# Performance work log

Measured on AMD Instinct MI355X. Metric: run time of the kernel, lower is better.

The kernel has to match this reference:

```python
import jax, jax.numpy as jnp
import numpy as np

INTERMEDIATE = 11008  # weight.size(0)
HIDDEN = 4096         # weight.size(1)
REMAINED = 4403       # int(11008 * 0.4)
BATCH = 64


def setup_inputs() -> dict:
    key = jax.random.key(0)
    k1, k2, k3 = jax.random.split(key, 3)
    x = jax.random.normal(k1, (BATCH, 1, HIDDEN), dtype=jnp.float32)
    weight = jax.random.normal(k2, (INTERMEDIATE, HIDDEN), dtype=jnp.float32) * 0.02
    indices = jax.random.randint(k3, (REMAINED,), 0, INTERMEDIATE, dtype=jnp.int32)
    return {"x": x, "weight": weight, "indices": indices}


def reference(x, weight, indices):
    # Decode path of UpLayer.forward: gather the activation-predicted neuron
    # rows into filtered_W, then x @ filtered_W.T  -> [B, 1, REMAINED]
    filtered_w = weight[indices]                      # [REMAINED, HIDDEN]
    return jnp.einsum('bsh,nh->bsn', x, filtered_w)   # [B, 1, REMAINED]
```

## Files before the change

kernel.cpp:

```cpp
#include <hip/hip_runtime.h>
#include <hip/hip_bf16.h>


#define HIDDEN 4096
#define KSPLIT 8
#define KCHUNK (HIDDEN / KSPLIT)
#define KSTEPS (KCHUNK / 32)
#define BATCH  64
#define NTILE  32
#define XBF_OFF (16u << 20)

using short8  = __attribute__((ext_vector_type(8))) short;
using f32x4   = __attribute__((ext_vector_type(4))) float;

__device__ __forceinline__ short f2bf(float f) {
    __bf16 h = (__bf16)f;
    return __builtin_bit_cast(short, h);
}

__global__ __launch_bounds__(256) void cvt_x(
    const float* __restrict__ x, unsigned short* __restrict__ xbf)
{
    const int i = (blockIdx.x * 256 + threadIdx.x) * 8;
    f32x4 a = *(const f32x4*)(x + i);
    f32x4 b = *(const f32x4*)(x + i + 4);
    short8 h;
    h[0] = f2bf(a[0]); h[1] = f2bf(a[1]); h[2] = f2bf(a[2]); h[3] = f2bf(a[3]);
    h[4] = f2bf(b[0]); h[5] = f2bf(b[1]); h[6] = f2bf(b[2]); h[7] = f2bf(b[3]);
    *(short8*)(xbf + i) = h;
}

__global__ __launch_bounds__(256, 4) void up_gather_gemm(
    const float*          __restrict__ weight,
    const unsigned short* __restrict__ xbf,
    const int*            __restrict__ indices,
    float*                __restrict__ ws,
    int R)
{
    __shared__ unsigned short wlds[NTILE * KCHUNK];

    const int t    = threadIdx.x;
    const int lane = t & 63;
    const int wave = t >> 6;
    const int nl   = lane & 15;
    const int kg   = lane >> 4;
    const int nb   = blockIdx.x;
    const int kb   = blockIdx.y;

    {
        const int r   = t >> 3;
        const int c   = t & 7;
        const int n   = nb * NTILE + r;
        const int row = indices[n < R ? n : R - 1];
        const float* src = weight + (size_t)row * HIDDEN + kb * KCHUNK + c * 8;
        char* ldsrow = (char*)wlds + r * (KCHUNK * 2);
        const unsigned int swz = (unsigned int)((r & 7) << 4);
#pragma unroll
        for (int s = 0; s < 8; ++s) {
            f32x4 v0 = *(const f32x4*)(src + (size_t)s * 64);
            f32x4 v1 = *(const f32x4*)(src + (size_t)s * 64 + 4);
            short8 h;
            h[0] = f2bf(v0[0]); h[1] = f2bf(v0[1]); h[2] = f2bf(v0[2]); h[3] = f2bf(v0[3]);
            h[4] = f2bf(v1[0]); h[5] = f2bf(v1[1]); h[6] = f2bf(v1[2]); h[7] = f2bf(v1[3]);
            const unsigned int bc = (unsigned int)(c * 16 + s * 128);
            *(short8*)(ldsrow + (bc ^ swz)) = h;
        }
    }

    const unsigned short* xrow =
        xbf + (size_t)(wave * 16 + nl) * HIDDEN + kb * KCHUNK + kg * 8;
    short8 afr[KSTEPS];
#pragma unroll
    for (int ks = 0; ks < KSTEPS; ++ks)
        afr[ks] = *(const short8*)(xrow + ks * 32);

    __syncthreads();

    f32x4 acc0 = {0.f,0.f,0.f,0.f}, acc1 = {0.f,0.f,0.f,0.f};

#pragma unroll
    for (int ks = 0; ks < KSTEPS; ++ks) {
#pragma unroll
        for (int nf = 0; nf < 2; ++nf) {
            const int rr = nf * 16 + nl;
            const unsigned int bc =
                (unsigned int)(ks * 64 + kg * 16) ^ (unsigned int)((rr & 7) << 4);
            short8 b = *(const short8*)((const char*)wlds + rr * (KCHUNK * 2) + bc);
            f32x4& acc = nf == 0 ? acc0 : acc1;
            acc = __builtin_amdgcn_mfma_f32_16x16x32_bf16(afr[ks], b, acc, 0, 0, 0);
        }
    }

    float* part = ws + (size_t)kb * BATCH * R;
    f32x4 accs[2] = {acc0, acc1};
#pragma unroll
    for (int nf = 0; nf < 2; ++nf) {
        const int nn = nb * NTILE + nf * 16 + nl;
        if (nn < R) {
#pragma unroll
            for (int r = 0; r < 4; ++r) {
                const int brow = wave * 16 + kg * 4 + r;
                part[(size_t)brow * R + nn] = accs[nf][r];
            }
        }
    }
}

__global__ __launch_bounds__(256) void reduce_partials(
    const float* __restrict__ ws, float* __restrict__ out, int n4, int stride4)
{
    const int i = blockIdx.x * blockDim.x + threadIdx.x;
    if (i >= n4) return;
    const f32x4* w = (const f32x4*)ws;
    f32x4 s = w[i];
#pragma unroll
    for (int kb = 1; kb < KSPLIT; ++kb) {
        f32x4 v = w[(size_t)kb * stride4 + i];
        s[0] += v[0]; s[1] += v[1]; s[2] += v[2]; s[3] += v[3];
    }
    ((f32x4*)out)[i] = s;
}

extern "C" void kernel_launch(void* const* d_in, const int* in_sizes, int n_in,
                              void* d_out, int out_size, void* d_ws, size_t ws_size,
                              hipStream_t stream) {
    const float* x       = (const float*)d_in[0];
    const float* weight  = (const float*)d_in[1];
    const int*   indices = (const int*)d_in[2];
    float*       out     = (float*)d_out;
    float*       ws      = (float*)d_ws;
    unsigned short* xbf  = (unsigned short*)((char*)d_ws + XBF_OFF);

    const int R  = in_sizes[2];
    const int nb = (R + NTILE - 1) / NTILE;

    cvt_x<<<dim3((BATCH * HIDDEN) / (256 * 8)), dim3(256), 0, stream>>>(x, xbf);
    up_gather_gemm<<<dim3(nb, KSPLIT), dim3(256), 0, stream>>>(weight, xbf, indices, ws, R);

    const int n4 = (BATCH * R) / 4;
    reduce_partials<<<dim3((n4 + 255) / 256), dim3(256), 0, stream>>>(ws, out, n4, n4);
}
```

Measured before the change: 32.45 us.

## Halve K-split and software-pipeline two K sub-chunks through registers

KSPLIT goes from 8 to 4, so each block covers 1024 K elements, processed as two 512-wide sub-chunks. The second sub-chunk's weight loads are issued into registers before the first chunk's MFMAs, overlapping global latency with compute. Halving the split also halves the partial-sum workspace that reduce_partials reads. The cost is fewer blocks (half the grid), higher register pressure (launch bounds lowered to 2), and an extra barrier pair.

```diff
diff --git a/kernel.cpp b/kernel.cpp
--- a/kernel.cpp
+++ b/kernel.cpp
@@ -3,19 +3,27 @@
 
 
 #define HIDDEN 4096
-#define KSPLIT 8
+#define KSPLIT 4
 #define KCHUNK (HIDDEN / KSPLIT)
-#define KSTEPS (KCHUNK / 32)
+#define SUB    512
+#define SSTEPS (SUB / 32)
 #define BATCH  64
 #define NTILE  32
 #define XBF_OFF (16u << 20)
 
-using short8  = __attribute__((ext_vector_type(8))) short;
-using f32x4   = __attribute__((ext_vector_type(4))) float;
+using short8 = __attribute__((ext_vector_type(8))) short;
+using f32x4  = __attribute__((ext_vector_type(4))) float;
 
 __device__ __forceinline__ short f2bf(float f) {
     __bf16 h = (__bf16)f;
     return __builtin_bit_cast(short, h);
+}
+
+__device__ __forceinline__ short8 cvt8(const f32x4& lo, const f32x4& hi) {
+    short8 r;
+    r[0] = f2bf(lo[0]); r[1] = f2bf(lo[1]); r[2] = f2bf(lo[2]); r[3] = f2bf(lo[3]);
+    r[4] = f2bf(hi[0]); r[5] = f2bf(hi[1]); r[6] = f2bf(hi[2]); r[7] = f2bf(hi[3]);
+    return r;
 }
 
 __global__ __launch_bounds__(256) void cvt_x(
@@ -24,20 +32,17 @@
     const int i = (blockIdx.x * 256 + threadIdx.x) * 8;
     f32x4 a = *(const f32x4*)(x + i);
     f32x4 b = *(const f32x4*)(x + i + 4);
-    short8 h;
-    h[0] = f2bf(a[0]); h[1] = f2bf(a[1]); h[2] = f2bf(a[2]); h[3] = f2bf(a[3]);
-    h[4] = f2bf(b[0]); h[5] = f2bf(b[1]); h[6] = f2bf(b[2]); h[7] = f2bf(b[3]);
-    *(short8*)(xbf + i) = h;
+    *(short8*)(xbf + i) = cvt8(a, b);
 }
 
-__global__ __launch_bounds__(256, 4) void up_gather_gemm(
+__global__ __launch_bounds__(256, 2) void gather_gemm(
     const float*          __restrict__ weight,
     const unsigned short* __restrict__ xbf,
     const int*            __restrict__ indices,
     float*                __restrict__ ws,
     int R)
 {
-    __shared__ unsigned short wlds[NTILE * KCHUNK];
+    __shared__ unsigned short wlds[NTILE * SUB];
 
     const int t    = threadIdx.x;
     const int lane = t & 63;
@@ -46,46 +51,80 @@
     const int kg   = lane >> 4;
     const int nb   = blockIdx.x;
     const int kb   = blockIdx.y;
+    const int k0   = kb * KCHUNK;
 
-    {
-        const int r   = t >> 3;
-        const int c   = t & 7;
-        const int n   = nb * NTILE + r;
-        const int row = indices[n < R ? n : R - 1];
-        const float* src = weight + (size_t)row * HIDDEN + kb * KCHUNK + c * 8;
-        char* ldsrow = (char*)wlds + r * (KCHUNK * 2);
-        const unsigned int swz = (unsigned int)((r & 7) << 4);
+    const int sr = t >> 3;
+    const int sc = t & 7;
+    const int ns = nb * NTILE + sr;
+    const int wrow = indices[ns < R ? ns : R - 1];
+    const float* wsrc = weight + (size_t)wrow * HIDDEN + k0 + sc * 8;
+    char* ldsrow = (char*)wlds + sr * (SUB * 2);
+    const unsigned int swz = (unsigned int)((sr & 7) << 4);
+
+    f32x4 sreg[16];
+
 #pragma unroll
-        for (int s = 0; s < 8; ++s) {
-            f32x4 v0 = *(const f32x4*)(src + (size_t)s * 64);
-            f32x4 v1 = *(const f32x4*)(src + (size_t)s * 64 + 4);
-            short8 h;
-            h[0] = f2bf(v0[0]); h[1] = f2bf(v0[1]); h[2] = f2bf(v0[2]); h[3] = f2bf(v0[3]);
-            h[4] = f2bf(v1[0]); h[5] = f2bf(v1[1]); h[6] = f2bf(v1[2]); h[7] = f2bf(v1[3]);
-            const unsigned int bc = (unsigned int)(c * 16 + s * 128);
-            *(short8*)(ldsrow + (bc ^ swz)) = h;
-        }
+    for (int s = 0; s < 8; ++s) {
+        sreg[2*s]   = *(const f32x4*)(wsrc + s * 64);
+        sreg[2*s+1] = *(const f32x4*)(wsrc + s * 64 + 4);
+    }
+#pragma unroll
+    for (int s = 0; s < 8; ++s) {
+        short8 h = cvt8(sreg[2*s], sreg[2*s+1]);
+        *(short8*)(ldsrow + ((unsigned int)(sc * 16 + s * 128) ^ swz)) = h;
     }
 
     const unsigned short* xrow =
-        xbf + (size_t)(wave * 16 + nl) * HIDDEN + kb * KCHUNK + kg * 8;
-    short8 afr[KSTEPS];
+        xbf + (size_t)(wave * 16 + nl) * HIDDEN + k0 + kg * 8;
+    short8 afr[SSTEPS];
 #pragma unroll
-    for (int ks = 0; ks < KSTEPS; ++ks)
+    for (int ks = 0; ks < SSTEPS; ++ks)
         afr[ks] = *(const short8*)(xrow + ks * 32);
 
     __syncthreads();
 
+#pragma unroll
+    for (int s = 0; s < 8; ++s) {
+        sreg[2*s]   = *(const f32x4*)(wsrc + SUB + s * 64);
+        sreg[2*s+1] = *(const f32x4*)(wsrc + SUB + s * 64 + 4);
+    }
+
     f32x4 acc0 = {0.f,0.f,0.f,0.f}, acc1 = {0.f,0.f,0.f,0.f};
 
 #pragma unroll
-    for (int ks = 0; ks < KSTEPS; ++ks) {
+    for (int ks = 0; ks < SSTEPS; ++ks) {
 #pragma unroll
         for (int nf = 0; nf < 2; ++nf) {
             const int rr = nf * 16 + nl;
             const unsigned int bc =
                 (unsigned int)(ks * 64 + kg * 16) ^ (unsigned int)((rr & 7) << 4);
-            short8 b = *(const short8*)((const char*)wlds + rr * (KCHUNK * 2) + bc);
+            short8 b = *(const short8*)((const char*)wlds + rr * (SUB * 2) + bc);
+            f32x4& acc = nf == 0 ? acc0 : acc1;
+            acc = __builtin_amdgcn_mfma_f32_16x16x32_bf16(afr[ks], b, acc, 0, 0, 0);
+        }
+    }
+
+    __syncthreads();
+
+#pragma unroll
+    for (int s = 0; s < 8; ++s) {
+        short8 h = cvt8(sreg[2*s], sreg[2*s+1]);
+        *(short8*)(ldsrow + ((unsigned int)(sc * 16 + s * 128) ^ swz)) = h;
+    }
+#pragma unroll
+    for (int ks = 0; ks < SSTEPS; ++ks)
+        afr[ks] = *(const short8*)(xrow + SUB + ks * 32);
+
+    __syncthreads();
+
+#pragma unroll
+    for (int ks = 0; ks < SSTEPS; ++ks) {
+#pragma unroll
+        for (int nf = 0; nf < 2; ++nf) {
+            const int rr = nf * 16 + nl;
+            const unsigned int bc =
+                (unsigned int)(ks * 64 + kg * 16) ^ (unsigned int)((rr & 7) << 4);
+            short8 b = *(const short8*)((const char*)wlds + rr * (SUB * 2) + bc);
             f32x4& acc = nf == 0 ? acc0 : acc1;
             acc = __builtin_amdgcn_mfma_f32_16x16x32_bf16(afr[ks], b, acc, 0, 0, 0);
         }
@@ -135,7 +174,7 @@
     const int nb = (R + NTILE - 1) / NTILE;
 
     cvt_x<<<dim3((BATCH * HIDDEN) / (256 * 8)), dim3(256), 0, stream>>>(x, xbf);
-    up_gather_gemm<<<dim3(nb, KSPLIT), dim3(256), 0, stream>>>(weight, xbf, indices, ws, R);
+    gather_gemm<<<dim3(nb, KSPLIT), dim3(256), 0, stream>>>(weight, xbf, indices, ws, R);
 
     const int n4 = (BATCH * R) / 4;
     reduce_partials<<<dim3((n4 + 255) / 256), dim3(256), 0, stream>>>(ws, out, n4, n4);
```

After: 34.94 us. 7.7% more time.

## Gather weight rows directly into LDS as fp32 via global_load_lds

Applied to the files above, without the earlier changes.

Weight rows are now copied straight from global memory into LDS as fp32 using the direct global-to-LDS load builtin, with the swizzle applied on the source address. Each row is loaded by one wave, and the conversion to bf16 moves to the MFMA loop at read time. This skips the register staging and the conversion before the LDS store, but doubles the LDS footprint to 64KB, so the occupancy hint drops from 4 blocks to 2. The reduce kernel also switches its partial-sum reads to nontemporal loads.

```diff
diff --git a/kernel.cpp b/kernel.cpp
--- a/kernel.cpp
+++ b/kernel.cpp
@@ -10,12 +10,22 @@
 #define NTILE  32
 #define XBF_OFF (16u << 20)
 
-using short8  = __attribute__((ext_vector_type(8))) short;
-using f32x4   = __attribute__((ext_vector_type(4))) float;
+using short8 = __attribute__((ext_vector_type(8))) short;
+using f32x4  = __attribute__((ext_vector_type(4))) float;
+
+typedef const void __attribute__((address_space(1))) gvoid;
+typedef void __attribute__((address_space(3))) svoid;
 
 __device__ __forceinline__ short f2bf(float f) {
     __bf16 h = (__bf16)f;
     return __builtin_bit_cast(short, h);
+}
+
+__device__ __forceinline__ short8 cvt8(const f32x4& lo, const f32x4& hi) {
+    short8 r;
+    r[0] = f2bf(lo[0]); r[1] = f2bf(lo[1]); r[2] = f2bf(lo[2]); r[3] = f2bf(lo[3]);
+    r[4] = f2bf(hi[0]); r[5] = f2bf(hi[1]); r[6] = f2bf(hi[2]); r[7] = f2bf(hi[3]);
+    return r;
 }
 
 __global__ __launch_bounds__(256) void cvt_x(
@@ -24,20 +34,17 @@
     const int i = (blockIdx.x * 256 + threadIdx.x) * 8;
     f32x4 a = *(const f32x4*)(x + i);
     f32x4 b = *(const f32x4*)(x + i + 4);
-    short8 h;
-    h[0] = f2bf(a[0]); h[1] = f2bf(a[1]); h[2] = f2bf(a[2]); h[3] = f2bf(a[3]);
-    h[4] = f2bf(b[0]); h[5] = f2bf(b[1]); h[6] = f2bf(b[2]); h[7] = f2bf(b[3]);
-    *(short8*)(xbf + i) = h;
+    *(short8*)(xbf + i) = cvt8(a, b);
 }
 
-__global__ __launch_bounds__(256, 4) void up_gather_gemm(
+__global__ __launch_bounds__(256, 2) void gather_gemm(
     const float*          __restrict__ weight,
     const unsigned short* __restrict__ xbf,
     const int*            __restrict__ indices,
     float*                __restrict__ ws,
     int R)
 {
-    __shared__ unsigned short wlds[NTILE * KCHUNK];
+    __shared__ float wlds[NTILE * KCHUNK];
 
     const int t    = threadIdx.x;
     const int lane = t & 63;
@@ -46,29 +53,31 @@
     const int kg   = lane >> 4;
     const int nb   = blockIdx.x;
     const int kb   = blockIdx.y;
+    const int k0   = kb * KCHUNK;
 
     {
-        const int r   = t >> 3;
-        const int c   = t & 7;
-        const int n   = nb * NTILE + r;
-        const int row = indices[n < R ? n : R - 1];
-        const float* src = weight + (size_t)row * HIDDEN + kb * KCHUNK + c * 8;
-        char* ldsrow = (char*)wlds + r * (KCHUNK * 2);
-        const unsigned int swz = (unsigned int)((r & 7) << 4);
+        const int r0 = wave * 8;
 #pragma unroll
-        for (int s = 0; s < 8; ++s) {
-            f32x4 v0 = *(const f32x4*)(src + (size_t)s * 64);
-            f32x4 v1 = *(const f32x4*)(src + (size_t)s * 64 + 4);
-            short8 h;
-            h[0] = f2bf(v0[0]); h[1] = f2bf(v0[1]); h[2] = f2bf(v0[2]); h[3] = f2bf(v0[3]);
-            h[4] = f2bf(v1[0]); h[5] = f2bf(v1[1]); h[6] = f2bf(v1[2]); h[7] = f2bf(v1[3]);
-            const unsigned int bc = (unsigned int)(c * 16 + s * 128);
-            *(short8*)(ldsrow + (bc ^ swz)) = h;
+        for (int j = 0; j < 8; ++j) {
+            const int r = r0 + j;
+            const int n = nb * NTILE + r;
+            const int wrow = indices[n < R ? n : R - 1];
+            const char* rowp = (const char*)(weight + (size_t)wrow * HIDDEN + k0);
+            const unsigned int swz = (unsigned int)((r & 7) << 4);
+#pragma unroll
+            for (int h = 0; h < 2; ++h) {
+                const unsigned int srcoff =
+                    ((unsigned int)(h * 1024 + lane * 16)) ^ swz;
+                __builtin_amdgcn_global_load_lds(
+                    (gvoid*)(rowp + srcoff),
+                    (svoid*)((char*)wlds + r * 2048 + h * 1024),
+                    16, 0, 0);
+            }
         }
     }
 
     const unsigned short* xrow =
-        xbf + (size_t)(wave * 16 + nl) * HIDDEN + kb * KCHUNK + kg * 8;
+        xbf + (size_t)(wave * 16 + nl) * HIDDEN + k0 + kg * 8;
     short8 afr[KSTEPS];
 #pragma unroll
     for (int ks = 0; ks < KSTEPS; ++ks)
@@ -83,9 +92,12 @@
 #pragma unroll
         for (int nf = 0; nf < 2; ++nf) {
             const int rr = nf * 16 + nl;
-            const unsigned int bc =
-                (unsigned int)(ks * 64 + kg * 16) ^ (unsigned int)((rr & 7) << 4);
-            short8 b = *(const short8*)((const char*)wlds + rr * (KCHUNK * 2) + bc);
+            const unsigned int swz = (unsigned int)((rr & 7) << 4);
+            const unsigned int g0 = (unsigned int)(ks * 128 + kg * 32);
+            const char* rowbase = (const char*)wlds + rr * 2048;
+            f32x4 w0 = *(const f32x4*)(rowbase + (g0 ^ swz));
+            f32x4 w1 = *(const f32x4*)(rowbase + ((g0 + 16) ^ swz));
+            short8 b = cvt8(w0, w1);
             f32x4& acc = nf == 0 ? acc0 : acc1;
             acc = __builtin_amdgcn_mfma_f32_16x16x32_bf16(afr[ks], b, acc, 0, 0, 0);
         }
@@ -112,10 +124,10 @@
     const int i = blockIdx.x * blockDim.x + threadIdx.x;
     if (i >= n4) return;
     const f32x4* w = (const f32x4*)ws;
-    f32x4 s = w[i];
+    f32x4 s = __builtin_nontemporal_load(&w[i]);
 #pragma unroll
     for (int kb = 1; kb < KSPLIT; ++kb) {
-        f32x4 v = w[(size_t)kb * stride4 + i];
+        f32x4 v = __builtin_nontemporal_load(&w[(size_t)kb * stride4 + i]);
         s[0] += v[0]; s[1] += v[1]; s[2] += v[2]; s[3] += v[3];
     }
     ((f32x4*)out)[i] = s;
@@ -135,7 +147,7 @@
     const int nb = (R + NTILE - 1) / NTILE;
 
     cvt_x<<<dim3((BATCH * HIDDEN) / (256 * 8)), dim3(256), 0, stream>>>(x, xbf);
-    up_gather_gemm<<<dim3(nb, KSPLIT), dim3(256), 0, stream>>>(weight, xbf, indices, ws, R);
+    gather_gemm<<<dim3(nb, KSPLIT), dim3(256), 0, stream>>>(weight, xbf, indices, ws, R);
 
     const int n4 = (BATCH * R) / 4;
     reduce_partials<<<dim3((n4 + 255) / 256), dim3(256), 0, stream>>>(ws, out, n4, n4);
```

Result: slower. 34.59 us (+6.6%).

## Fuse x conversion, gather GEMM and split-K reduction into one cooperative kernel

Applied to the files above, without the earlier changes.

Replaces the three launches (x to bf16 conversion, gather GEMM, partial reduction) with a single persistent cooperative kernel. Each block loops over tile/k-chunk work items, converts fp32 x to bf16 in registers right before the MFMA, and after a grid-wide sync reduces the split-K partials itself. This is meant to remove two kernel launch gaps and the bf16 x buffer round trip. In exchange it adds a grid sync, re-converts x once per work item, and hardcodes the tile count at 138, which ties the kernel to R=4403.

```diff
diff --git a/kernel.cpp b/kernel.cpp
--- a/kernel.cpp
+++ b/kernel.cpp
@@ -1,5 +1,8 @@
 #include <hip/hip_runtime.h>
 #include <hip/hip_bf16.h>
+#include <hip/hip_cooperative_groups.h>
+
+namespace cg = cooperative_groups;
 
 
 #define HIDDEN 4096
@@ -8,33 +11,30 @@
 #define KSTEPS (KCHUNK / 32)
 #define BATCH  64
 #define NTILE  32
-#define XBF_OFF (16u << 20)
+#define NTILES 138
+#define WORK   (NTILES * KSPLIT)
 
-using short8  = __attribute__((ext_vector_type(8))) short;
-using f32x4   = __attribute__((ext_vector_type(4))) float;
+using short8 = __attribute__((ext_vector_type(8))) short;
+using f32x4  = __attribute__((ext_vector_type(4))) float;
 
 __device__ __forceinline__ short f2bf(float f) {
     __bf16 h = (__bf16)f;
     return __builtin_bit_cast(short, h);
 }
 
-__global__ __launch_bounds__(256) void cvt_x(
-    const float* __restrict__ x, unsigned short* __restrict__ xbf)
-{
-    const int i = (blockIdx.x * 256 + threadIdx.x) * 8;
-    f32x4 a = *(const f32x4*)(x + i);
-    f32x4 b = *(const f32x4*)(x + i + 4);
-    short8 h;
-    h[0] = f2bf(a[0]); h[1] = f2bf(a[1]); h[2] = f2bf(a[2]); h[3] = f2bf(a[3]);
-    h[4] = f2bf(b[0]); h[5] = f2bf(b[1]); h[6] = f2bf(b[2]); h[7] = f2bf(b[3]);
-    *(short8*)(xbf + i) = h;
+__device__ __forceinline__ short8 cvt8(const f32x4& lo, const f32x4& hi) {
+    short8 r;
+    r[0] = f2bf(lo[0]); r[1] = f2bf(lo[1]); r[2] = f2bf(lo[2]); r[3] = f2bf(lo[3]);
+    r[4] = f2bf(hi[0]); r[5] = f2bf(hi[1]); r[6] = f2bf(hi[2]); r[7] = f2bf(hi[3]);
+    return r;
 }
 
-__global__ __launch_bounds__(256, 4) void up_gather_gemm(
-    const float*          __restrict__ weight,
-    const unsigned short* __restrict__ xbf,
-    const int*            __restrict__ indices,
-    float*                __restrict__ ws,
+__global__ __launch_bounds__(256, 4) void fused_up(
+    const float* __restrict__ weight,
+    const float* __restrict__ x,
+    const int*   __restrict__ indices,
+    float*       __restrict__ part,
+    float*       __restrict__ out,
     int R)
 {
     __shared__ unsigned short wlds[NTILE * KCHUNK];
@@ -44,81 +44,80 @@
     const int wave = t >> 6;
     const int nl   = lane & 15;
     const int kg   = lane >> 4;
-    const int nb   = blockIdx.x;
-    const int kb   = blockIdx.y;
+    const int sr   = t >> 3;
+    const int sc   = t & 7;
 
-    {
-        const int r   = t >> 3;
-        const int c   = t & 7;
-        const int n   = nb * NTILE + r;
-        const int row = indices[n < R ? n : R - 1];
-        const float* src = weight + (size_t)row * HIDDEN + kb * KCHUNK + c * 8;
-        char* ldsrow = (char*)wlds + r * (KCHUNK * 2);
-        const unsigned int swz = (unsigned int)((r & 7) << 4);
+    for (int wk = blockIdx.x; wk < WORK; wk += gridDim.x) {
+        const int kb = wk / NTILES;
+        const int nb = wk - kb * NTILES;
+        const int k0 = kb * KCHUNK;
+
+        __syncthreads();
+
+        {
+            const int n    = nb * NTILE + sr;
+            const int wrow = indices[n < R ? n : R - 1];
+            const float* src = weight + (size_t)wrow * HIDDEN + k0 + sc * 8;
+            char* ldsrow = (char*)wlds + sr * (KCHUNK * 2);
+            const unsigned int swz = (unsigned int)((sr & 7) << 4);
 #pragma unroll
-        for (int s = 0; s < 8; ++s) {
-            f32x4 v0 = *(const f32x4*)(src + (size_t)s * 64);
-            f32x4 v1 = *(const f32x4*)(src + (size_t)s * 64 + 4);
-            short8 h;
-            h[0] = f2bf(v0[0]); h[1] = f2bf(v0[1]); h[2] = f2bf(v0[2]); h[3] = f2bf(v0[3]);
-            h[4] = f2bf(v1[0]); h[5] = f2bf(v1[1]); h[6] = f2bf(v1[2]); h[7] = f2bf(v1[3]);
-            const unsigned int bc = (unsigned int)(c * 16 + s * 128);
-            *(short8*)(ldsrow + (bc ^ swz)) = h;
+            for (int s = 0; s < 8; ++s) {
+                f32x4 v0 = *(const f32x4*)(src + s * 64);
+                f32x4 v1 = *(const f32x4*)(src + s * 64 + 4);
+                short8 h = cvt8(v0, v1);
+                *(short8*)(ldsrow + ((unsigned int)(sc * 16 + s * 128) ^ swz)) = h;
+            }
+        }
+        __syncthreads();
+
+        const float* xrow = x + (size_t)(wave * 16 + nl) * HIDDEN + k0 + kg * 8;
+        f32x4 acc0 = {0.f,0.f,0.f,0.f}, acc1 = {0.f,0.f,0.f,0.f};
+
+#pragma unroll
+        for (int ks = 0; ks < KSTEPS; ++ks) {
+            f32x4 xa = *(const f32x4*)(xrow + ks * 32);
+            f32x4 xb = *(const f32x4*)(xrow + ks * 32 + 4);
+            short8 a = cvt8(xa, xb);
+#pragma unroll
+            for (int nf = 0; nf < 2; ++nf) {
+                const int rr = nf * 16 + nl;
+                const unsigned int bc =
+                    (unsigned int)(ks * 64 + kg * 16) ^ (unsigned int)((rr & 7) << 4);
+                short8 b = *(const short8*)((const char*)wlds + rr * (KCHUNK * 2) + bc);
+                f32x4& acc = nf == 0 ? acc0 : acc1;
+                acc = __builtin_amdgcn_mfma_f32_16x16x32_bf16(a, b, acc, 0, 0, 0);
+            }
+        }
+
+        float* p = part + (size_t)kb * BATCH * R;
+        f32x4 accs[2] = {acc0, acc1};
+#pragma unroll
+        for (int nf = 0; nf < 2; ++nf) {
+            const int nn = nb * NTILE + nf * 16 + nl;
+            if (nn < R) {
+#pragma unroll
+                for (int r = 0; r < 4; ++r) {
+                    const int brow = wave * 16 + kg * 4 + r;
+                    p[(size_t)brow * R + nn] = accs[nf][r];
+                }
+            }
         }
     }
 
-    const unsigned short* xrow =
-        xbf + (size_t)(wave * 16 + nl) * HIDDEN + kb * KCHUNK + kg * 8;
-    short8 afr[KSTEPS];
+    cg::this_grid().sync();
+
+    const int n4 = (BATCH * R) / 4;
+    const int T  = gridDim.x * 256;
+    const f32x4* pw = (const f32x4*)part;
+    for (int i = blockIdx.x * 256 + t; i < n4; i += T) {
+        f32x4 s = pw[i];
 #pragma unroll
-    for (int ks = 0; ks < KSTEPS; ++ks)
-        afr[ks] = *(const short8*)(xrow + ks * 32);
-
-    __syncthreads();
-
-    f32x4 acc0 = {0.f,0.f,0.f,0.f}, acc1 = {0.f,0.f,0.f,0.f};
-
-#pragma unroll
-    for (int ks = 0; ks < KSTEPS; ++ks) {
-#pragma unroll
-        for (int nf = 0; nf < 2; ++nf) {
-            const int rr = nf * 16 + nl;
-            const unsigned int bc =
-                (unsigned int)(ks * 64 + kg * 16) ^ (unsigned int)((rr & 7) << 4);
-            short8 b = *(const short8*)((const char*)wlds + rr * (KCHUNK * 2) + bc);
-            f32x4& acc = nf == 0 ? acc0 : acc1;
-            acc = __builtin_amdgcn_mfma_f32_16x16x32_bf16(afr[ks], b, acc, 0, 0, 0);
+        for (int kb = 1; kb < KSPLIT; ++kb) {
+            f32x4 v = pw[(size_t)kb * n4 + i];
+            s[0] += v[0]; s[1] += v[1]; s[2] += v[2]; s[3] += v[3];
         }
+        ((f32x4*)out)[i] = s;
     }
-
-    float* part = ws + (size_t)kb * BATCH * R;
-    f32x4 accs[2] = {acc0, acc1};
-#pragma unroll
-    for (int nf = 0; nf < 2; ++nf) {
-        const int nn = nb * NTILE + nf * 16 + nl;
-        if (nn < R) {
-#pragma unroll
-            for (int r = 0; r < 4; ++r) {
-                const int brow = wave * 16 + kg * 4 + r;
-                part[(size_t)brow * R + nn] = accs[nf][r];
-            }
-        }
-    }
-}
-
-__global__ __launch_bounds__(256) void reduce_partials(
-    const float* __restrict__ ws, float* __restrict__ out, int n4, int stride4)
-{
-    const int i = blockIdx.x * blockDim.x + threadIdx.x;
-    if (i >= n4) return;
-    const f32x4* w = (const f32x4*)ws;
-    f32x4 s = w[i];
-#pragma unroll
-    for (int kb = 1; kb < KSPLIT; ++kb) {
-        f32x4 v = w[(size_t)kb * stride4 + i];
-        s[0] += v[0]; s[1] += v[1]; s[2] += v[2]; s[3] += v[3];
-    }
-    ((f32x4*)out)[i] = s;
 }
 
 extern "C" void kernel_launch(void* const* d_in, const int* in_sizes, int n_in,
@@ -128,15 +127,17 @@
     const float* weight  = (const float*)d_in[1];
     const int*   indices = (const int*)d_in[2];
     float*       out     = (float*)d_out;
-    float*       ws      = (float*)d_ws;
-    unsigned short* xbf  = (unsigned short*)((char*)d_ws + XBF_OFF);
+    float*       part    = (float*)d_ws;
+    int          R       = in_sizes[2];
 
-    const int R  = in_sizes[2];
-    const int nb = (R + NTILE - 1) / NTILE;
+    int perCU = 0;
+    if (hipOccupancyMaxActiveBlocksPerMultiprocessor(&perCU, fused_up, 256, 0)
+            != hipSuccess || perCU <= 0)
+        perCU = 2;
+    int G = perCU * 256;
+    if (G > WORK) G = WORK;
 
-    cvt_x<<<dim3((BATCH * HIDDEN) / (256 * 8)), dim3(256), 0, stream>>>(x, xbf);
-    up_gather_gemm<<<dim3(nb, KSPLIT), dim3(256), 0, stream>>>(weight, xbf, indices, ws, R);
-
-    const int n4 = (BATCH * R) / 4;
-    reduce_partials<<<dim3((n4 + 255) / 256), dim3(256), 0, stream>>>(ws, out, n4, n4);
+    void* args[] = {(void*)&weight, (void*)&x, (void*)&indices,
+                    (void*)&part, (void*)&out, (void*)&R};
+    hipLaunchCooperativeKernel((void*)fused_up, dim3(G), dim3(256), args, 0, stream);
 }
```

New measurement: 122.9 us. 279% more time.
